# Kernel tuning notes

Measured on AMD Instinct MI355X. Metric: run time of the kernel, lower is better.

Reference implementation:

```python
import jax, jax.numpy as jnp
import numpy as np

N_NODES = 50000
N_EDGES = 600000
HID = 128
OUT = 14
LAYERS = 3
N_GRAPHS = 16
NODE_VOCAB = (120, 6)
EDGE_VOCAB = (6, 3)
GEN_EPS = 1e-7   # GENConv eps added after ReLU on messages
BN_EPS = 1e-5    # torch BatchNorm1d default eps


def setup_inputs() -> dict:
    key = jax.random.key(0)
    ks = jax.random.split(key, 14)
    inp = {}
    inp['node_feat0'] = jax.random.randint(ks[0], (N_NODES,), 0, NODE_VOCAB[0], dtype=jnp.int32)
    inp['node_feat1'] = jax.random.randint(ks[1], (N_NODES,), 0, NODE_VOCAB[1], dtype=jnp.int32)
    inp['edge_feat0'] = jax.random.randint(ks[2], (N_EDGES,), 0, EDGE_VOCAB[0], dtype=jnp.int32)
    inp['edge_feat1'] = jax.random.randint(ks[3], (N_EDGES,), 0, EDGE_VOCAB[1], dtype=jnp.int32)
    inp['edge_src'] = jax.random.randint(ks[4], (N_EDGES,), 0, N_NODES, dtype=jnp.int32)
    inp['edge_dst'] = jax.random.randint(ks[5], (N_EDGES,), 0, N_NODES, dtype=jnp.int32)
    inp['graph_ids'] = jnp.repeat(jnp.arange(N_GRAPHS, dtype=jnp.int32), N_NODES // N_GRAPHS)
    inp['num_graphs'] = N_GRAPHS
    s = 0.05
    inp['W_node0'] = jax.random.normal(ks[6], (NODE_VOCAB[0], HID), jnp.float32) * s
    inp['W_node1'] = jax.random.normal(ks[7], (NODE_VOCAB[1], HID), jnp.float32) * s
    # per-layer edge embedding tables (each GENConv layer has its own)
    inp['edge_emb0'] = jax.random.normal(ks[8], (LAYERS, EDGE_VOCAB[0], HID), jnp.float32) * s
    inp['edge_emb1'] = jax.random.normal(ks[9], (LAYERS, EDGE_VOCAB[1], HID), jnp.float32) * s
    inp['beta'] = jnp.ones((LAYERS,), jnp.float32)  # learnable softmax temperature, init 1.0
    inp['mlp_W'] = jax.random.normal(ks[10], (LAYERS, HID, HID), jnp.float32) * (1.0 / np.sqrt(HID))
    inp['mlp_b'] = jnp.zeros((LAYERS, HID), jnp.float32)
    inp['bn_gamma'] = jnp.ones((LAYERS, HID), jnp.float32)
    inp['bn_beta'] = jnp.zeros((LAYERS, HID), jnp.float32)
    inp['W_out'] = jax.random.normal(ks[11], (HID, OUT), jnp.float32) * (1.0 / np.sqrt(HID))
    inp['b_out'] = jnp.zeros((OUT,), jnp.float32)
    return inp


def _segment_softmax(z, seg, num_segments):
    # DGL edge_softmax: elementwise softmax over edges sharing a destination node.
    zmax = jax.ops.segment_max(z, seg, num_segments=num_segments)
    zmax = jnp.where(jnp.isfinite(zmax), zmax, 0.0)  # guard empty segments
    e = jnp.exp(z - zmax[seg])
    denom = jax.ops.segment_sum(e, seg, num_segments=num_segments)
    return e / denom[seg]


def reference(node_feat0, node_feat1, edge_feat0, edge_feat1, edge_src, edge_dst,
              graph_ids, num_graphs, W_node0, W_node1, edge_emb0, edge_emb1,
              beta, mlp_W, mlp_b, bn_gamma, bn_beta, W_out, b_out):
    # node embedding lookup + sum over tables
    hv = W_node0[node_feat0] + W_node1[node_feat1]          # [N, H]
    n = hv.shape[0]
    for l in range(mlp_W.shape[0]):
        # BatchNorm1d (training mode: batch stats, biased variance) + ReLU
        mu = jnp.mean(hv, axis=0)
        var = jnp.var(hv, axis=0)
        hv1 = (hv - mu) * jax.lax.rsqrt(var + BN_EPS) * bn_gamma[l] + bn_beta[l]
        hv1 = jax.nn.relu(hv1)
        # GENConv: edge embed sum, u_add_e, relu+eps, edge_softmax, scatter-sum
        ee = edge_emb0[l][edge_feat0] + edge_emb1[l][edge_feat1]   # [E, H]
        m = jax.nn.relu(hv1[edge_src] + ee) + GEN_EPS              # [E, H]
        a = _segment_softmax(m * beta[l], edge_dst, n)             # [E, H]
        agg = jax.ops.segment_sum(m * a, edge_dst, num_segments=n)  # [N, H]
        # feats = node_feats + msg, then 1-layer MLP, then outer skip connect
        hv = (hv1 + agg) @ mlp_W[l] + mlp_b[l] + hv
    # AvgPooling over each graph in the batch, then output Linear
    counts = jax.ops.segment_sum(jnp.ones((n,), hv.dtype), graph_ids, num_segments=num_graphs)
    hg = jax.ops.segment_sum(hv, graph_ids, num_segments=num_graphs) / counts[:, None]
    return hg @ W_out + b_out  # [num_graphs, OUT]
```

## Files before the change

### kernel.cpp

```cpp
#include <hip/hip_runtime.h>

#define N_NODESC 50000
#define N_EDGESC 600000
#define HID 128
#define LAYERS 3
#define N_GRAPHSC 16
#define OUT_DIM 14
#define GEN_EPS 1e-7f
#define BN_EPS 1e-5f
#define SCAN_BLK 196
#define EMB_BLK 6250
#define WF_BLK 192
#define CNT_BLK 2344
#define GEMM_BLK 782
#define BNR_BLK 64
#define EDGE_CAP 1792
#define LOG2E 1.44269504f

typedef short bf16x8 __attribute__((ext_vector_type(8)));
typedef float f32x4 __attribute__((ext_vector_type(4)));

__device__ __forceinline__ unsigned short f2bf(float f) {
    union { float f; unsigned u; } v; v.f = f;
    unsigned r = v.u + 0x7FFF + ((v.u >> 16) & 1);
    return (unsigned short)(r >> 16);
}
__device__ __forceinline__ float bf_lo(unsigned u) {
    return __uint_as_float(u << 16);
}
__device__ __forceinline__ float bf_hi(unsigned u) {
    return __uint_as_float(u & 0xFFFF0000u);
}
__device__ __forceinline__ float bfs(unsigned short u) {
    return __uint_as_float(((unsigned)u) << 16);
}

__global__ void k_blocksum(const int* __restrict__ deg, int* __restrict__ part) {
    __shared__ int sh[256];
    int t = threadIdx.x;
    int i = blockIdx.x * 256 + t;
    sh[t] = (i < N_NODESC) ? deg[i] : 0;
    __syncthreads();
    for (int off = 128; off > 0; off >>= 1) {
        if (t < off) sh[t] += sh[t + off];
        __syncthreads();
    }
    if (t == 0) part[blockIdx.x] = sh[0];
}

__global__ void k_scanpart(const int* __restrict__ part, int* __restrict__ bofs) {
    __shared__ int sh[256];
    int t = threadIdx.x;
    int v = (t < SCAN_BLK) ? part[t] : 0;
    sh[t] = v;
    __syncthreads();
    for (int off = 1; off < 256; off <<= 1) {
        int add = (t >= off) ? sh[t - off] : 0;
        __syncthreads();
        sh[t] += add;
        __syncthreads();
    }
    if (t < SCAN_BLK) bofs[t] = sh[t] - v;
}

__global__ void k_rowptr(const int* __restrict__ deg, const int* __restrict__ bofs,
                         int* __restrict__ row_ptr, int* __restrict__ cursor) {
    __shared__ int sh[256];
    int t = threadIdx.x;
    int i = blockIdx.x * 256 + t;
    int d = (i < N_NODESC) ? deg[i] : 0;
    sh[t] = d;
    __syncthreads();
    for (int off = 1; off < 256; off <<= 1) {
        int add = (t >= off) ? sh[t - off] : 0;
        __syncthreads();
        sh[t] += add;
        __syncthreads();
    }
    if (i < N_NODESC) {
        int rp = bofs[blockIdx.x] + sh[t] - d;
        row_ptr[i] = rp;
        cursor[i] = rp;
    }
    if (i == 0) row_ptr[N_NODESC] = N_EDGESC;
}

__global__ void k_scatter(const int* __restrict__ dst, const int* __restrict__ src,
                          const int* __restrict__ f0, const int* __restrict__ f1,
                          int* __restrict__ cursor, int* __restrict__ csr_pack) {
    int i = blockIdx.x * blockDim.x + threadIdx.x;
    if (i < N_EDGESC) {
        int pos = atomicAdd(&cursor[dst[i]], 1);
        csr_pack[pos] = (src[i] << 8) | ((f0[i] * 3 + f1[i]) * 8);
    }
}

__global__ void k_embed(const int* __restrict__ f0, const int* __restrict__ f1,
                        const float4* __restrict__ W0, const float4* __restrict__ W1,
                        uint2* __restrict__ hvb2, float* __restrict__ part,
                        const float* __restrict__ W, unsigned short* __restrict__ wf,
                        const int* __restrict__ edst, int* __restrict__ deg) {
    int tid = threadIdx.x;
    if (blockIdx.x >= EMB_BLK + WF_BLK) {
        int e = (blockIdx.x - EMB_BLK - WF_BLK) * 256 + tid;
        if (e < N_EDGESC) atomicAdd(&deg[edst[e]], 1);
        return;
    }
    if (blockIdx.x >= EMB_BLK) {
        int i = (blockIdx.x - EMB_BLK) * 256 + tid;
        if (i < LAYERS * 16384) {
            int j = i & 7;
            int lane = (i >> 3) & 63;
            int nt = (i >> 9) & 7;
            int ks = (i >> 12) & 3;
            int l = i >> 14;
            int k = ks * 32 + (lane >> 4) * 8 + j;
            int n = nt * 16 + (lane & 15);
            wf[i] = f2bf(W[(size_t)l * HID * HID + k * HID + n]);
        }
        return;
    }
    __shared__ float sh[1024], sh2[1024];
    int i = blockIdx.x * 256 + tid;
    int v = i >> 5, c4 = i & 31;
    float4 a = W0[f0[v] * 32 + c4];
    float4 b = W1[f1[v] * 32 + c4];
    float4 o = make_float4(a.x + b.x, a.y + b.y, a.z + b.z, a.w + b.w);
    uint2 ob;
    ob.x = (unsigned)f2bf(o.x) | ((unsigned)f2bf(o.y) << 16);
    ob.y = (unsigned)f2bf(o.z) | ((unsigned)f2bf(o.w) << 16);
    hvb2[i] = ob;
    sh[tid * 4 + 0] = o.x; sh2[tid * 4 + 0] = o.x * o.x;
    sh[tid * 4 + 1] = o.y; sh2[tid * 4 + 1] = o.y * o.y;
    sh[tid * 4 + 2] = o.z; sh2[tid * 4 + 2] = o.z * o.z;
    sh[tid * 4 + 3] = o.w; sh2[tid * 4 + 3] = o.w * o.w;
    __syncthreads();
    if (tid < 128) {
        int c4i = tid >> 2, j = tid & 3;
        float s = 0.f, s2 = 0.f;
#pragma unroll
        for (int r = 0; r < 8; r++) {
            s += sh[(r * 32 + c4i) * 4 + j];
            s2 += sh2[(r * 32 + c4i) * 4 + j];
        }
        part[(size_t)blockIdx.x * 256 + tid] = s;
        part[(size_t)blockIdx.x * 256 + 128 + tid] = s2;
    }
}

__global__ void k_bn_reduce2(const float* __restrict__ part, int nparts,
                             float* __restrict__ gsum) {
    int t = threadIdx.x;
    int rows = (nparts + BNR_BLK - 1) / BNR_BLK;
    int r0 = blockIdx.x * rows;
    int r1 = min(r0 + rows, nparts);
    float s = 0.f;
    for (int p = r0; p < r1; p++) s += part[(size_t)p * 256 + t];
    atomicAdd(&gsum[t], s);
}

__global__ __launch_bounds__(1024) void k_aggemm(
    const unsigned* __restrict__ hin, unsigned short* __restrict__ hout,
    const int* __restrict__ row_ptr, const int* __restrict__ csr_pack,
    const float* __restrict__ e0, const float* __restrict__ e1,
    const float* __restrict__ beta_p, const unsigned short* __restrict__ wf,
    const float* __restrict__ b, const float* __restrict__ gsum,
    const float* __restrict__ gamma, const float* __restrict__ betab,
    float* __restrict__ gsum_next, float* __restrict__ hg) {
    __shared__ float2 sh_et[18 * 64];
    __shared__ unsigned x_tile[64 * 64];
    __shared__ float shs[512], shs2[512];
    __shared__ int sh_pack[EDGE_CAP];
    __shared__ int sh_rp[65];
    __shared__ int row_ctr;
    int tid = threadIdx.x;
    for (int i = tid; i < 18 * 64; i += 1024) {
        int f = i >> 6, ln = i & 63;
        int a = f / 3, bb = f - 3 * a;
        float2 ea = *(const float2*)(e0 + a * HID + 2 * ln);
        float2 eb = *(const float2*)(e1 + bb * HID + 2 * ln);
        sh_et[i] = make_float2(ea.x + eb.x, ea.y + eb.y);
    }
    int w = tid >> 6, lane = tid & 63;
    int m0 = blockIdx.x * 64;
    if (tid < 65) sh_rp[tid] = row_ptr[min(m0 + tid, N_NODESC)];
    if (tid == 0) row_ctr = 0;
    int eb0 = row_ptr[m0];
    int eb1 = row_ptr[min(m0 + 64, N_NODESC)];
    int nE = min(eb1 - eb0, EDGE_CAP);
    for (int i = tid; i < nE; i += 1024) sh_pack[i] = csr_pack[eb0 + i];

    const float bl2 = (*beta_p) * LOG2E;
    const float invN = 1.f / (float)N_NODESC;
    int cch = lane * 2;
    float mu0 = gsum[cch] * invN, mu1 = gsum[cch + 1] * invN;
    float var0 = gsum[128 + cch] * invN - mu0 * mu0;
    float var1 = gsum[129 + cch] * invN - mu1 * mu1;
    float sc0 = gamma[cch] * rsqrtf(var0 + BN_EPS);
    float sc1 = gamma[cch + 1] * rsqrtf(var1 + BN_EPS);
    float sf0 = betab[cch] - mu0 * sc0;
    float sf1 = betab[cch + 1] - mu1 * sc1;
    __syncthreads();

    const char* hinc = (const char*)hin;
    const char* etc = (const char*)sh_et;
    unsigned lane4 = (unsigned)lane * 4;
    unsigned lane8 = (unsigned)lane * 8;

#define GATH(S, PK)                                                         \
    unsigned u##S = *(const unsigned*)(hinc +                               \
                        ((((unsigned)(PK)) & 0xFFFFFF00u) + lane4));        \
    float2 t##S = *(const float2*)(etc +                                    \
                        (((((unsigned)(PK)) & 0xFFu) << 6) + lane8));
#define CMP(S, VAL)                                                         \
    {                                                                       \
        float a0 = fmaxf(fmaf(bf_lo(u##S), sc0, sf0), 0.f);                 \
        float a1 = fmaxf(fmaf(bf_hi(u##S), sc1, sf1), 0.f);                 \
        float r0 = fmaxf(a0 + t##S.x, 0.f);                                 \
        float r1 = fmaxf(a1 + t##S.y, 0.f);                                 \
        float ei0 = (VAL) ? (r0 * bl2) : -1000.f;                           \
        float ei1 = (VAL) ? (r1 * bl2) : -1000.f;                           \
        float w0 = exp2f(ei0);                                              \
        float w1 = exp2f(ei1);                                              \
        d0 += w0; d1 += w1;                                                 \
        n0 = fmaf(r0, w0, n0); n1 = fmaf(r1, w1, n1);                       \
    }
#define EDGE_LOOP(SRC)                                                      \
    for (int j0 = 0; j0 < deg; j0 += 4) {                                   \
        int i0 = p0 + j0;                                                   \
        int pkA = SRC(i0);                                                  \
        int pkB = SRC(min(i0 + 1, last));                                   \
        int pkC = SRC(min(i0 + 2, last));                                   \
        int pkD = SRC(min(i0 + 3, last));                                   \
        GATH(A, pkA) GATH(B, pkB) GATH(C, pkC) GATH(D, pkD)                 \
        int rem = deg - j0;                                                 \
        CMP(A, true)                                                        \
        CMP(B, rem > 1)                                                     \
        CMP(C, rem > 2)                                                     \
        CMP(D, rem > 3)                                                     \
    }
#define SRC_LDS(I) sh_pack[(I)]
#define SRC_GLB(I) csr_pack[eb0 + (I)]

    for (;;) {
        int rsel = 0;
        if (lane == 0) rsel = atomicAdd(&row_ctr, 1);
        rsel = __builtin_amdgcn_readfirstlane(rsel);
        if (rsel >= 64) break;
        int row = rsel;
        int v = m0 + row;
        int vc = min(v, N_NODESC - 1);
        unsigned su = hin[(size_t)vc * 64 + lane];
        float h10 = fmaxf(fmaf(bf_lo(su), sc0, sf0), 0.f);
        float h11 = fmaxf(fmaf(bf_hi(su), sc1, sf1), 0.f);
        int p0 = sh_rp[row] - eb0;
        int deg = sh_rp[row + 1] - sh_rp[row];
        int last = p0 + deg - 1;
        float n0 = 0.f, n1 = 0.f, d0 = 0.f, d1 = 0.f;
        if (p0 + deg <= nE) {
            EDGE_LOOP(SRC_LDS)
        } else {
            EDGE_LOOP(SRC_GLB)
        }
        float ox = h10 + (deg ? __fdividef(n0, d0) + GEN_EPS : 0.f);
        float oy = h11 + (deg ? __fdividef(n1, d1) + GEN_EPS : 0.f);
        x_tile[row * 64 + ((lane + row * 4) & 63)] =
            (unsigned)f2bf(ox) | ((unsigned)f2bf(oy) << 16);
    }
#undef EDGE_LOOP
#undef GATH
#undef CMP
#undef SRC_LDS
#undef SRC_GLB
    __syncthreads();

    int rw = w & 3, chh = w >> 2;
    int mrow = lane & 15, grp = lane >> 4;
    int rbase = rw * 16 + mrow;
    bf16x8 af[4];
#pragma unroll
    for (int ks = 0; ks < 4; ks++) {
        int col = ks * 16 + grp * 4;
        int colr = (col + rbase * 4) & 63;
        af[ks] = *(const bf16x8*)&x_tile[rbase * 64 + colr];
    }
    f32x4 acc[2];
#pragma unroll
    for (int nt = 0; nt < 2; nt++) acc[nt] = (f32x4){0.f, 0.f, 0.f, 0.f};
#pragma unroll
    for (int nt = 0; nt < 2; nt++) {
        int ntg = chh * 2 + nt;
#pragma unroll
        for (int ks = 0; ks < 4; ks++) {
            bf16x8 bfr = *(const bf16x8*)(wf +
                (size_t)((ks * 8 + ntg) * 64 + lane) * 8);
            acc[nt] = __builtin_amdgcn_mfma_f32_16x16x32_bf16(
                af[ks], bfr, acc[nt], 0, 0, 0);
        }
    }
    const unsigned short* hin_s = (const unsigned short*)hin;
    int gA = m0 / 3125;
    int boundary = (gA + 1) * 3125;
#pragma unroll
    for (int nt = 0; nt < 2; nt++) {
        int col = chh * 32 + nt * 16 + mrow;
        float bias = b[col];
        float s = 0.f, s2 = 0.f;
#pragma unroll
        for (int r = 0; r < 4; r++) {
            int v = m0 + rw * 16 + grp * 4 + r;
            if (v < N_NODESC) {
                size_t idx = (size_t)v * HID + col;
                float o = acc[nt][r] + bias + bfs(hin_s[idx]);
                hout[idx] = f2bf(o);
                if (hg) {
                    if (v < boundary) s += o; else s2 += o;
                } else {
                    s += o; s2 += o * o;
                }
            }
        }
        s  += __shfl_xor(s, 16, 64);  s  += __shfl_xor(s, 32, 64);
        s2 += __shfl_xor(s2, 16, 64); s2 += __shfl_xor(s2, 32, 64);
        if (lane < 16) { shs[rw * 128 + col] = s; shs2[rw * 128 + col] = s2; }
    }
    __syncthreads();
    if (hg) {
        int gB = min(m0 + 63, N_NODESC - 1) / 3125;
        if (tid < 128) {
            atomicAdd(&hg[gA * 128 + tid],
                shs[tid] + shs[128 + tid] + shs[256 + tid] + shs[384 + tid]);
        } else if (tid < 256 && gB != gA) {
            int c = tid - 128;
            atomicAdd(&hg[gB * 128 + c],
                shs2[c] + shs2[128 + c] + shs2[256 + c] + shs2[384 + c]);
        }
    } else if (gsum_next) {
        if (tid < 128) {
            atomicAdd(&gsum_next[tid],
                shs[tid] + shs[128 + tid] + shs[256 + tid] + shs[384 + tid]);
        } else if (tid < 256) {
            int c = tid - 128;
            atomicAdd(&gsum_next[tid],
                shs2[c] + shs2[128 + c] + shs2[256 + c] + shs2[384 + c]);
        }
    }
}

__global__ void k_finish(const float* __restrict__ hg, const float* __restrict__ Wo,
                         const float* __restrict__ bo, float* __restrict__ out) {
    int t = threadIdx.x;
    if (t >= N_GRAPHSC * OUT_DIM) return;
    int g = t / OUT_DIM, o = t % OUT_DIM;
    const float inv = (float)N_GRAPHSC / (float)N_NODESC;
    float acc = bo[o];
    for (int k = 0; k < HID; k++)
        acc += hg[g * HID + k] * inv * Wo[k * OUT_DIM + o];
    out[t] = acc;
}

extern "C" void kernel_launch(void* const* d_in, const int* in_sizes, int n_in,
                              void* d_out, int out_size, void* d_ws, size_t ws_size,
                              hipStream_t stream) {
    const int* node_feat0 = (const int*)d_in[0];
    const int* node_feat1 = (const int*)d_in[1];
    const int* edge_feat0 = (const int*)d_in[2];
    const int* edge_feat1 = (const int*)d_in[3];
    const int* edge_src   = (const int*)d_in[4];
    const int* edge_dst   = (const int*)d_in[5];
    const float* W_node0   = (const float*)d_in[8];
    const float* W_node1   = (const float*)d_in[9];
    const float* edge_emb0 = (const float*)d_in[10];
    const float* edge_emb1 = (const float*)d_in[11];
    const float* beta      = (const float*)d_in[12];
    const float* mlp_W     = (const float*)d_in[13];
    const float* mlp_b     = (const float*)d_in[14];
    const float* bn_gamma  = (const float*)d_in[15];
    const float* bn_beta   = (const float*)d_in[16];
    const float* W_out     = (const float*)d_in[17];
    const float* b_out     = (const float*)d_in[18];
    float* out = (float*)d_out;

    char* ws = (char*)d_ws;
    size_t off = 0;
    auto alloc = [&](size_t bytes) -> void* {
        void* p = ws + off;
        off += (bytes + 255) & ~(size_t)255;
        return p;
    };
    unsigned short* hvA = (unsigned short*)alloc((size_t)N_NODESC * HID * 2);
    unsigned short* hvB = (unsigned short*)alloc((size_t)N_NODESC * HID * 2);
    float* gsums   = (float*)alloc(LAYERS * 256 * 4);
    float* hg      = (float*)alloc(N_GRAPHSC * HID * 4);
    float* bnpart  = (float*)alloc((size_t)EMB_BLK * 256 * 4);
    unsigned short* wfrag = (unsigned short*)alloc((size_t)LAYERS * 16384 * 2);
    int* row_ptr   = (int*)alloc((N_NODESC + 1) * 4);
    int* cursor    = (int*)alloc(N_NODESC * 4);
    int* deg       = (int*)alloc(N_NODESC * 4);
    int* part      = (int*)alloc(SCAN_BLK * 4);
    int* bofs      = (int*)alloc(SCAN_BLK * 4);
    int* csr_pack  = (int*)alloc((size_t)N_EDGESC * 4);

    hipMemsetAsync(deg, 0, N_NODESC * 4, stream);
    hipMemsetAsync(gsums, 0, LAYERS * 256 * 4 + N_GRAPHSC * HID * 4, stream);

    k_embed<<<EMB_BLK + WF_BLK + CNT_BLK, 256, 0, stream>>>(
        node_feat0, node_feat1, (const float4*)W_node0, (const float4*)W_node1,
        (uint2*)hvA, bnpart, mlp_W, wfrag, edge_dst, deg);

    k_blocksum<<<SCAN_BLK, 256, 0, stream>>>(deg, part);
    k_scanpart<<<1, 256, 0, stream>>>(part, bofs);
    k_rowptr<<<SCAN_BLK, 256, 0, stream>>>(deg, bofs, row_ptr, cursor);
    k_scatter<<<(N_EDGESC + 255) / 256, 256, 0, stream>>>(
        edge_dst, edge_src, edge_feat0, edge_feat1, cursor, csr_pack);

    k_bn_reduce2<<<BNR_BLK, 256, 0, stream>>>(bnpart, EMB_BLK, gsums);

    unsigned short* hin = hvA;
    unsigned short* hout = hvB;
    for (int l = 0; l < LAYERS; l++) {
        float* gsum = gsums + l * 256;
        float* gnext = (l + 1 < LAYERS) ? gsums + (l + 1) * 256 : nullptr;
        float* hgp = (l == LAYERS - 1) ? hg : nullptr;
        k_aggemm<<<GEMM_BLK, 1024, 0, stream>>>(
            (const unsigned*)hin, hout, row_ptr, csr_pack,
            edge_emb0 + (size_t)l * 6 * HID, edge_emb1 + (size_t)l * 3 * HID,
            beta + l, wfrag + (size_t)l * 16384, mlp_b + l * HID,
            gsum, bn_gamma + l * HID, bn_beta + l * HID, gnext, hgp);
        unsigned short* tmp = hin; hin = hout; hout = tmp;
    }

    k_finish<<<1, 256, 0, stream>>>(hg, W_out, b_out, out);
}
```

Measured before the change: 383.0 us.

## Fuse CSR scan and BN reduction into one kernel with atomic block offsets

Replaces the three-kernel prefix scan (blocksum, scanpart, rowptr) with one kernel. Each 256-node block takes its base offset from a global atomic counter, so blocks may be laid out in any order. The BN partial-sum reduction runs as extra blocks of that same kernel, spread over more blocks, which cuts launches and serial dependencies. The aggregation kernel now reads per-node degree instead of row_ptr[i+1] to handle the non-monotonic block order. The LDS edge buffer is zero-padded so the fast path can drop its index clamps, at the cost of a nondeterministic CSR edge order.

```diff
diff --git a/kernel.cpp b/kernel.cpp
--- a/kernel.cpp
+++ b/kernel.cpp
@@ -13,7 +13,7 @@
 #define WF_BLK 192
 #define CNT_BLK 2344
 #define GEMM_BLK 782
-#define BNR_BLK 64
+#define BNR_BLK 512
 #define EDGE_CAP 1792
 #define LOG2E 1.44269504f
 
@@ -35,24 +35,25 @@
     return __uint_as_float(((unsigned)u) << 16);
 }
 
-__global__ void k_blocksum(const int* __restrict__ deg, int* __restrict__ part) {
+__global__ void k_csrbn(const int* __restrict__ deg, const float* __restrict__ part,
+                        int* __restrict__ row_ptr, int* __restrict__ cursor,
+                        int* __restrict__ gctr, float* __restrict__ gsum) {
+    int t = threadIdx.x;
+    if (blockIdx.x >= SCAN_BLK) {
+        int b = blockIdx.x - SCAN_BLK;
+        const int rows = (EMB_BLK + BNR_BLK - 1) / BNR_BLK;
+        int r0 = b * rows;
+        int r1 = min(r0 + rows, EMB_BLK);
+        float s = 0.f;
+        for (int p = r0; p < r1; p++) s += part[(size_t)p * 256 + t];
+        atomicAdd(&gsum[t], s);
+        return;
+    }
     __shared__ int sh[256];
-    int t = threadIdx.x;
+    __shared__ int sbase;
     int i = blockIdx.x * 256 + t;
-    sh[t] = (i < N_NODESC) ? deg[i] : 0;
-    __syncthreads();
-    for (int off = 128; off > 0; off >>= 1) {
-        if (t < off) sh[t] += sh[t + off];
-        __syncthreads();
-    }
-    if (t == 0) part[blockIdx.x] = sh[0];
-}
-
-__global__ void k_scanpart(const int* __restrict__ part, int* __restrict__ bofs) {
-    __shared__ int sh[256];
-    int t = threadIdx.x;
-    int v = (t < SCAN_BLK) ? part[t] : 0;
-    sh[t] = v;
+    int d = (i < N_NODESC) ? deg[i] : 0;
+    sh[t] = d;
     __syncthreads();
     for (int off = 1; off < 256; off <<= 1) {
         int add = (t >= off) ? sh[t - off] : 0;
@@ -60,29 +61,13 @@
         sh[t] += add;
         __syncthreads();
     }
-    if (t < SCAN_BLK) bofs[t] = sh[t] - v;
-}
-
-__global__ void k_rowptr(const int* __restrict__ deg, const int* __restrict__ bofs,
-                         int* __restrict__ row_ptr, int* __restrict__ cursor) {
-    __shared__ int sh[256];
-    int t = threadIdx.x;
-    int i = blockIdx.x * 256 + t;
-    int d = (i < N_NODESC) ? deg[i] : 0;
-    sh[t] = d;
-    __syncthreads();
-    for (int off = 1; off < 256; off <<= 1) {
-        int add = (t >= off) ? sh[t - off] : 0;
-        __syncthreads();
-        sh[t] += add;
-        __syncthreads();
-    }
+    if (t == 255) sbase = atomicAdd(gctr, sh[255]);
+    __syncthreads();
     if (i < N_NODESC) {
-        int rp = bofs[blockIdx.x] + sh[t] - d;
+        int rp = sbase + sh[t] - d;
         row_ptr[i] = rp;
         cursor[i] = rp;
     }
-    if (i == 0) row_ptr[N_NODESC] = N_EDGESC;
 }
 
 __global__ void k_scatter(const int* __restrict__ dst, const int* __restrict__ src,
@@ -148,20 +133,10 @@
     }
 }
 
-__global__ void k_bn_reduce2(const float* __restrict__ part, int nparts,
-                             float* __restrict__ gsum) {
-    int t = threadIdx.x;
-    int rows = (nparts + BNR_BLK - 1) / BNR_BLK;
-    int r0 = blockIdx.x * rows;
-    int r1 = min(r0 + rows, nparts);
-    float s = 0.f;
-    for (int p = r0; p < r1; p++) s += part[(size_t)p * 256 + t];
-    atomicAdd(&gsum[t], s);
-}
-
 __global__ __launch_bounds__(1024) void k_aggemm(
     const unsigned* __restrict__ hin, unsigned short* __restrict__ hout,
-    const int* __restrict__ row_ptr, const int* __restrict__ csr_pack,
+    const int* __restrict__ row_ptr, const int* __restrict__ degp,
+    const int* __restrict__ csr_pack,
     const float* __restrict__ e0, const float* __restrict__ e1,
     const float* __restrict__ beta_p, const unsigned short* __restrict__ wf,
     const float* __restrict__ b, const float* __restrict__ gsum,
@@ -170,8 +145,9 @@
     __shared__ float2 sh_et[18 * 64];
     __shared__ unsigned x_tile[64 * 64];
     __shared__ float shs[512], shs2[512];
-    __shared__ int sh_pack[EDGE_CAP];
-    __shared__ int sh_rp[65];
+    __shared__ int sh_pack[EDGE_CAP + 8];
+    __shared__ int sh_rp[64];
+    __shared__ int sh_deg[64];
     __shared__ int row_ctr;
     int tid = threadIdx.x;
     for (int i = tid; i < 18 * 64; i += 1024) {
@@ -183,12 +159,17 @@
     }
     int w = tid >> 6, lane = tid & 63;
     int m0 = blockIdx.x * 64;
-    if (tid < 65) sh_rp[tid] = row_ptr[min(m0 + tid, N_NODESC)];
+    if (tid < 64) {
+        int v = m0 + tid;
+        sh_rp[tid] = row_ptr[min(v, N_NODESC - 1)];
+        sh_deg[tid] = (v < N_NODESC) ? degp[v] : 0;
+    }
     if (tid == 0) row_ctr = 0;
     int eb0 = row_ptr[m0];
-    int eb1 = row_ptr[min(m0 + 64, N_NODESC)];
-    int nE = min(eb1 - eb0, EDGE_CAP);
+    int rl = min(m0 + 63, N_NODESC - 1);
+    int nE = min(row_ptr[rl] + degp[rl] - eb0, EDGE_CAP);
     for (int i = tid; i < nE; i += 1024) sh_pack[i] = csr_pack[eb0 + i];
+    if (tid < 8) sh_pack[nE + tid] = 0;
 
     const float bl2 = (*beta_p) * LOG2E;
     const float invN = 1.f / (float)N_NODESC;
@@ -225,22 +206,6 @@
         d0 += w0; d1 += w1;                                                 \
         n0 = fmaf(r0, w0, n0); n1 = fmaf(r1, w1, n1);                       \
     }
-#define EDGE_LOOP(SRC)                                                      \
-    for (int j0 = 0; j0 < deg; j0 += 4) {                                   \
-        int i0 = p0 + j0;                                                   \
-        int pkA = SRC(i0);                                                  \
-        int pkB = SRC(min(i0 + 1, last));                                   \
-        int pkC = SRC(min(i0 + 2, last));                                   \
-        int pkD = SRC(min(i0 + 3, last));                                   \
-        GATH(A, pkA) GATH(B, pkB) GATH(C, pkC) GATH(D, pkD)                 \
-        int rem = deg - j0;                                                 \
-        CMP(A, true)                                                        \
-        CMP(B, rem > 1)                                                     \
-        CMP(C, rem > 2)                                                     \
-        CMP(D, rem > 3)                                                     \
-    }
-#define SRC_LDS(I) sh_pack[(I)]
-#define SRC_GLB(I) csr_pack[eb0 + (I)]
 
     for (;;) {
         int rsel = 0;
@@ -254,24 +219,45 @@
         float h10 = fmaxf(fmaf(bf_lo(su), sc0, sf0), 0.f);
         float h11 = fmaxf(fmaf(bf_hi(su), sc1, sf1), 0.f);
         int p0 = sh_rp[row] - eb0;
-        int deg = sh_rp[row + 1] - sh_rp[row];
-        int last = p0 + deg - 1;
+        int deg = sh_deg[row];
         float n0 = 0.f, n1 = 0.f, d0 = 0.f, d1 = 0.f;
         if (p0 + deg <= nE) {
-            EDGE_LOOP(SRC_LDS)
+            for (int j0 = 0; j0 < deg; j0 += 4) {
+                int i0 = p0 + j0;
+                int pkA = sh_pack[i0];
+                int pkB = sh_pack[i0 + 1];
+                int pkC = sh_pack[i0 + 2];
+                int pkD = sh_pack[i0 + 3];
+                GATH(A, pkA) GATH(B, pkB) GATH(C, pkC) GATH(D, pkD)
+                int rem = deg - j0;
+                CMP(A, true)
+                CMP(B, rem > 1)
+                CMP(C, rem > 2)
+                CMP(D, rem > 3)
+            }
         } else {
-            EDGE_LOOP(SRC_GLB)
+            int last = p0 + deg - 1;
+            for (int j0 = 0; j0 < deg; j0 += 4) {
+                int i0 = p0 + j0;
+                int pkA = csr_pack[eb0 + i0];
+                int pkB = csr_pack[eb0 + min(i0 + 1, last)];
+                int pkC = csr_pack[eb0 + min(i0 + 2, last)];
+                int pkD = csr_pack[eb0 + min(i0 + 3, last)];
+                GATH(A, pkA) GATH(B, pkB) GATH(C, pkC) GATH(D, pkD)
+                int rem = deg - j0;
+                CMP(A, true)
+                CMP(B, rem > 1)
+                CMP(C, rem > 2)
+                CMP(D, rem > 3)
+            }
         }
         float ox = h10 + (deg ? __fdividef(n0, d0) + GEN_EPS : 0.f);
         float oy = h11 + (deg ? __fdividef(n1, d1) + GEN_EPS : 0.f);
         x_tile[row * 64 + ((lane + row * 4) & 63)] =
             (unsigned)f2bf(ox) | ((unsigned)f2bf(oy) << 16);
     }
-#undef EDGE_LOOP
 #undef GATH
 #undef CMP
-#undef SRC_LDS
-#undef SRC_GLB
     __syncthreads();
 
     int rw = w & 3, chh = w >> 2;
@@ -392,29 +378,26 @@
     unsigned short* hvB = (unsigned short*)alloc((size_t)N_NODESC * HID * 2);
     float* gsums   = (float*)alloc(LAYERS * 256 * 4);
     float* hg      = (float*)alloc(N_GRAPHSC * HID * 4);
+    int*   gctr    = (int*)alloc(256);
     float* bnpart  = (float*)alloc((size_t)EMB_BLK * 256 * 4);
     unsigned short* wfrag = (unsigned short*)alloc((size_t)LAYERS * 16384 * 2);
     int* row_ptr   = (int*)alloc((N_NODESC + 1) * 4);
     int* cursor    = (int*)alloc(N_NODESC * 4);
     int* deg       = (int*)alloc(N_NODESC * 4);
-    int* part      = (int*)alloc(SCAN_BLK * 4);
-    int* bofs      = (int*)alloc(SCAN_BLK * 4);
-    int* csr_pack  = (int*)alloc((size_t)N_EDGESC * 4);
+    int* csr_pack  = (int*)alloc((size_t)N_EDGESC * 4 + 64);
 
     hipMemsetAsync(deg, 0, N_NODESC * 4, stream);
-    hipMemsetAsync(gsums, 0, LAYERS * 256 * 4 + N_GRAPHSC * HID * 4, stream);
+    hipMemsetAsync(gsums, 0, LAYERS * 256 * 4 + N_GRAPHSC * HID * 4 + 256, stream);
 
     k_embed<<<EMB_BLK + WF_BLK + CNT_BLK, 256, 0, stream>>>(
         node_feat0, node_feat1, (const float4*)W_node0, (const float4*)W_node1,
         (uint2*)hvA, bnpart, mlp_W, wfrag, edge_dst, deg);
 
-    k_blocksum<<<SCAN_BLK, 256, 0, stream>>>(deg, part);
-    k_scanpart<<<1, 256, 0, stream>>>(part, bofs);
-    k_rowptr<<<SCAN_BLK, 256, 0, stream>>>(deg, bofs, row_ptr, cursor);
+    k_csrbn<<<SCAN_BLK + BNR_BLK, 256, 0, stream>>>(
+        deg, bnpart, row_ptr, cursor, gctr, gsums);
+
     k_scatter<<<(N_EDGESC + 255) / 256, 256, 0, stream>>>(
         edge_dst, edge_src, edge_feat0, edge_feat1, cursor, csr_pack);
-
-    k_bn_reduce2<<<BNR_BLK, 256, 0, stream>>>(bnpart, EMB_BLK, gsums);
 
     unsigned short* hin = hvA;
     unsigned short* hout = hvB;
@@ -423,7 +406,7 @@
         float* gnext = (l + 1 < LAYERS) ? gsums + (l + 1) * 256 : nullptr;
         float* hgp = (l == LAYERS - 1) ? hg : nullptr;
         k_aggemm<<<GEMM_BLK, 1024, 0, stream>>>(
-            (const unsigned*)hin, hout, row_ptr, csr_pack,
+            (const unsigned*)hin, hout, row_ptr, deg, csr_pack,
             edge_emb0 + (size_t)l * 6 * HID, edge_emb1 + (size_t)l * 3 * HID,
             beta + l, wfrag + (size_t)l * 16384, mlp_b + l * HID,
             gsum, bn_gamma + l * HID, bn_beta + l * HID, gnext, hgp);
```

New measurement: 374.9 us. 1.02x faster.
